# Kernel tuning notes

Hardware: AMD Instinct MI355X
Metric: run time of the kernel (lower is better)

## Reference

```python
import jax, jax.numpy as jnp
import numpy as np

NC = 80          # num_classes
NA = 3           # anchors per scale
G = 1.0          # offset magnitude; 1 + ceil(G/0.5) = 3
THRESH = 4.0     # anchor wh ratio threshold
BALANCE = (4.0, 1.0, 0.4)
CP, CN = 1.0, 0.0  # smooth_BCE(eps=0.0)
ANCHORS = np.array([[10, 13], [16, 30], [33, 23],
                    [30, 61], [62, 45], [59, 119],
                    [116, 90], [156, 198], [373, 326]], np.float32).reshape(3, 3, 2)
OFFS = np.array([[0, 0], [1, 0], [0, 1], [-1, 0], [0, -1]], np.float32) * G


def _build_targets(targets, grids, image_size):
    """Host-side (numpy) YOLOv7 target assignment: per-scale offset expansion,
    in-grid filtering and anchor-ratio filtering (data-dependent shapes)."""
    tcls, tbox, indices, anch = [], [], [], []
    for i, (H, W) in enumerate(grids):
        ng = np.array([H, W], np.float32)
        stride = image_size / ng                 # [sy, sx]
        anchor = ANCHORS[i] / stride[[1, 0]]     # anchors (w,h) in grid units
        gain = np.ones(6, np.float32)
        gain[2:] = (1.0 / stride)[[1, 0, 1, 0]]  # scale cx,cy,w,h to grid units
        rows = (targets * gain).reshape(-1, 6)   # [M,6]: nb,cls,cx,cy,w,h
        nb_, cls_, cx, cy, gw, gh = rows.T
        gx = cx[None, :] - OFFS[:, 0:1]          # [5,M] candidate cell x
        gy = cy[None, :] - OFFS[:, 1:2]
        brd = lambda v: np.broadcast_to(v[None, :], gx.shape)
        cand = np.stack([brd(nb_), brd(cls_), brd(cx), brd(cy),
                         gx, gy, brd(gw), brd(gh)], -1)        # [5,M,8]
        j = (gx >= 0) & (gx < ng[1]) & (gy >= 0) & (gy < ng[0])
        t = cand[j]                                             # [K,8]
        r = t[None, :, 6:8] / anchor[:, None]                   # [na,K,2]
        jj = np.maximum(r, 1.0 / r).max(-1) < THRESH            # [na,K]
        ai = np.broadcast_to(np.arange(NA, dtype=np.float32)[:, None], jj.shape)
        t = np.concatenate([np.broadcast_to(t[None], (NA,) + t.shape)[jj],
                            ai[jj][:, None]], 1)                # [n,9]
        b = t[:, 0].astype(np.int64)
        c = t[:, 1].astype(np.int64)
        gij = t[:, 4:6].astype(np.int64)                        # (gi, gj)
        a = t[:, 8].astype(np.int64)
        indices.append((jnp.asarray(b), jnp.asarray(a),
                        jnp.asarray(gij[:, 1]), jnp.asarray(gij[:, 0])))
        tbox.append(jnp.asarray(np.concatenate([t[:, 2:4] - gij, t[:, 6:8]], 1)))
        anch.append(jnp.asarray(anchor[a]))
        tcls.append(jnp.asarray(c))
    return tcls, tbox, indices, anch


def _ciou(box1, box2, eps=1e-7):
    # boxes in cxcywh, shape [n,4]
    w1, h1 = box1[:, 2], box1[:, 3]
    w2, h2 = box2[:, 2], box2[:, 3]
    b1x1, b1x2 = box1[:, 0] - w1 / 2, box1[:, 0] + w1 / 2
    b1y1, b1y2 = box1[:, 1] - h1 / 2, box1[:, 1] + h1 / 2
    b2x1, b2x2 = box2[:, 0] - w2 / 2, box2[:, 0] + w2 / 2
    b2y1, b2y2 = box2[:, 1] - h2 / 2, box2[:, 1] + h2 / 2
    inter = (jnp.clip(jnp.minimum(b1x2, b2x2) - jnp.maximum(b1x1, b2x1), 0) *
             jnp.clip(jnp.minimum(b1y2, b2y2) - jnp.maximum(b1y1, b2y1), 0))
    union = w1 * h1 + w2 * h2 - inter + eps
    iou = inter / union
    cw = jnp.maximum(b1x2, b2x2) - jnp.minimum(b1x1, b2x1)
    ch = jnp.maximum(b1y2, b2y2) - jnp.minimum(b1y1, b2y1)
    c2 = cw ** 2 + ch ** 2 + eps
    rho2 = ((b2x1 + b2x2 - b1x1 - b1x2) ** 2 +
            (b2y1 + b2y2 - b1y1 - b1y2) ** 2) / 4.0
    v = (4.0 / jnp.pi ** 2) * (jnp.arctan(w2 / (h2 + eps)) -
                               jnp.arctan(w1 / (h1 + eps))) ** 2
    alpha = jax.lax.stop_gradient(v / (v - iou + (1.0 + eps)))
    return iou - (rho2 / c2 + v * alpha)


def _bce_logits(x, t):
    # mean-reduced BCEWithLogits (pos_weight=1)
    return jnp.mean(jnp.maximum(x, 0) - x * t + jnp.log1p(jnp.exp(-jnp.abs(x))))


def _loss(preds, targets_np, image_size_np):
    grids = [p.shape[-2:] for p in preds]
    tcls, tbox, indices, anch = _build_targets(targets_np, grids, image_size_np)
    lbox = jnp.float32(0.0)
    lobj = jnp.float32(0.0)
    lcls = jnp.float32(0.0)
    for i, pi in enumerate(preds):
        B, C, H, W = pi.shape
        p = pi.reshape(B, NA, C // NA, H, W).transpose(0, 1, 3, 4, 2)  # [B,na,H,W,no]
        b, a, gj, gi = indices[i]
        tobj = jnp.zeros(p.shape[:-1], p.dtype)
        n = int(b.shape[0])
        if n:
            ps = p[b, a, gj, gi]                                       # [n,no]
            pxy = jax.nn.sigmoid(ps[:, 0:2]) * 3.0 - G                 # (1+ceil(G/0.5))=3
            pwh = (jax.nn.sigmoid(ps[:, 2:4]) * 2.0) ** 2 * anch[i]
            iou = _ciou(jnp.concatenate([pxy, pwh], 1), tbox[i])
            lbox = lbox + (1.0 - iou).mean()
            tobj = tobj.at[b, a, gj, gi].set(
                jnp.clip(jax.lax.stop_gradient(iou), 0.0).astype(p.dtype))
            if NC > 1:
                t = jnp.full((n, NC), CN, p.dtype)
                t = t.at[jnp.arange(n), tcls[i] - 1].set(CP)
                lcls = lcls + _bce_logits(ps[:, 5:], t)
        lobj = lobj + _bce_logits(p[..., 4], tobj) * BALANCE[i]
    lbox, lobj, lcls = lbox * 3.54, lobj * 64.3, lcls * 37.4
    return lbox + lobj + lcls, lbox, lobj, lcls


def setup_inputs() -> dict:
    key = jax.random.key(0)
    k0, k1, k2, k3, k4, k5 = jax.random.split(key, 6)
    B, m = 16, 12
    p0 = jax.random.normal(k0, (B, 255, 80, 80), jnp.float32)
    p1 = jax.random.normal(k1, (B, 255, 40, 40), jnp.float32)
    p2 = jax.random.normal(k2, (B, 255, 20, 20), jnp.float32)
    nb = jnp.broadcast_to(jnp.arange(B, dtype=jnp.float32)[:, None], (B, m))
    cls = jax.random.randint(k3, (B, m), 1, NC + 1).astype(jnp.float32)
    cxy = jax.random.uniform(k4, (B, m, 2), jnp.float32, 0.05, 0.95)
    wh = jax.random.uniform(k5, (B, m, 2), jnp.float32, 0.02, 0.4)
    targets = jnp.concatenate([nb[..., None], cls[..., None], cxy, wh], -1)
    image_size = jnp.array([640.0, 640.0], jnp.float32)
    return {"p0": p0, "p1": p1, "p2": p2, "targets": targets, "image_size": image_size}


def reference(p0, p1, p2, targets, image_size):
    return _loss((p0, p1, p2), np.asarray(targets), np.asarray(image_size))
```

## Files before the change

kernel.cpp:

```cpp
#include <hip/hip_runtime.h>
#include <math.h>


#define NT     192
#define NOFF   5
#define NANCH  3
#define MAXC   (NANCH*NOFF*NT)
#define THRESH 4.0f
#define NB     16
#define NCLS   80
#define NPLANE 144
#define NBLK   (NPLANE + 3)
#define MAGIC  0x5EED0001
#define WS_FLAG   0
#define WS_DENSE  160
#define WS_ASSIGN 320

__device__ __constant__ int   c_H[3]  = {80, 40, 20};
__device__ __constant__ int   c_W[3]  = {80, 40, 20};
__device__ __constant__ int   c_HW[3] = {6400, 1600, 400};
__device__ __constant__ float c_anch[18] = {10,13, 16,30, 33,23,
                                            30,61, 62,45, 59,119,
                                            116,90, 156,198, 373,326};
__device__ __constant__ float c_offs[10] = {0,0, 1,0, 0,1, -1,0, 0,-1};

__device__ __forceinline__ float sigmoidf(float x) {
    return 1.0f / (1.0f + __expf(-x));
}
__device__ __forceinline__ float softplusf(float x) {
    return fmaxf(x, 0.0f) + __logf(1.0f + __expf(-fabsf(x)));
}

__global__ void __launch_bounds__(256)
k_fused(const float* __restrict__ p0,
        const float* __restrict__ p1,
        const float* __restrict__ p2,
        const float* __restrict__ targets,
        const float* __restrict__ image_size,
        float* __restrict__ ws,
        float* __restrict__ out) {
    const int bid = blockIdx.x;
    const int tid = threadIdx.x;
    int* iws = (int*)ws;

    __shared__ float s_red[8];
    __shared__ float s_t[NT * 6];
    __shared__ float s_isz[2];
    __shared__ float s_sp[3];

    if (tid < 8) s_red[tid] = 0.0f;
    if (tid < 3) s_sp[tid] = 0.0f;

    if (bid < NPLANE) {
        const int scale = bid / (NB * NANCH);
        const int rem   = bid % (NB * NANCH);
        const int b     = rem / NANCH;
        const int a     = rem % NANCH;
        const int HW    = c_HW[scale];
        const float* p  = (scale == 0) ? p0 : ((scale == 1) ? p1 : p2);
        const float4* plane = (const float4*)(p + (size_t)b * 255 * HW
                                                + (size_t)(a * 85 + 4) * HW);
        const int n4 = HW >> 2;
        float s = 0.0f;
        for (int i = tid; i < n4; i += 256) {
            const float4 v = plane[i];
            s += softplusf(v.x) + softplusf(v.y) + softplusf(v.z) + softplusf(v.w);
        }
        for (int off = 32; off > 0; off >>= 1) s += __shfl_down(s, off, 64);
        if ((tid & 63) == 0) s_red[tid >> 6] = s;
        __syncthreads();
        if (tid == 0) {
            const float part = s_red[0] + s_red[1] + s_red[2] + s_red[3];
            atomicExch(&ws[WS_DENSE + bid], part);
            __threadfence();
            atomicExch(&iws[WS_FLAG + bid], MAGIC);
        }
    } else {
        const int scale = bid - NPLANE;
        if (tid == 0) { s_isz[0] = image_size[0]; s_isz[1] = image_size[1]; }
        for (int k = tid; k < NT * 6; k += 256) s_t[k] = targets[k];
        __syncthreads();

        const int H = c_H[scale], W = c_W[scale];
        const int HW = c_HW[scale];
        const float gx_mul = (float)W / s_isz[1];
        const float gy_mul = (float)H / s_isz[0];
        const float* p = (scale == 0) ? p0 : ((scale == 1) ? p1 : p2);

        int   n_loc = 0;
        float corr_loc = 0.0f, lbox_loc = 0.0f, lcls_loc = 0.0f;

        for (int k = tid; k < MAXC; k += 256) {
            const int a   = k / (NOFF * NT);
            const int rm  = k % (NOFF * NT);
            const int o   = rm / NT;
            const int t   = rm % NT;

            const float cx = s_t[t*6 + 2] * gx_mul;
            const float cy = s_t[t*6 + 3] * gy_mul;
            const float gw = s_t[t*6 + 4] * gx_mul;
            const float gh = s_t[t*6 + 5] * gy_mul;

            const float gxf = cx - c_offs[o*2 + 0];
            const float gyf = cy - c_offs[o*2 + 1];
            if (!(gxf >= 0.0f && gxf < (float)W && gyf >= 0.0f && gyf < (float)H))
                continue;

            const float aw = c_anch[(scale*3 + a)*2 + 0] * gx_mul;
            const float ah = c_anch[(scale*3 + a)*2 + 1] * gy_mul;
            const float rx = gw / aw, ry = gh / ah;
            const float mr = fmaxf(fmaxf(rx, 1.0f/rx), fmaxf(ry, 1.0f/ry));
            if (!(mr < THRESH)) continue;

            n_loc++;

            const int b   = (int)s_t[t*6 + 0];
            const int cls = (int)s_t[t*6 + 1];
            const int gi  = (int)gxf;
            const int gj  = (int)gyf;
            const float tbx = cx - (float)gi;
            const float tby = cy - (float)gj;

            const float* base = p + (size_t)b * 255 * HW + (size_t)(a * 85) * HW
                                  + (size_t)gj * W + gi;

            const float ps0 = base[0];
            const float ps1 = base[(size_t)HW];
            const float ps2 = base[2*(size_t)HW];
            const float ps3 = base[3*(size_t)HW];
            const float ps4 = base[4*(size_t)HW];

            const float px = sigmoidf(ps0) * 3.0f - 1.0f;
            const float py = sigmoidf(ps1) * 3.0f - 1.0f;
            float pw = sigmoidf(ps2) * 2.0f; pw = pw * pw * aw;
            float ph = sigmoidf(ps3) * 2.0f; ph = ph * ph * ah;

            const float eps = 1e-7f;
            const float b1x1 = px - pw*0.5f, b1x2 = px + pw*0.5f;
            const float b1y1 = py - ph*0.5f, b1y2 = py + ph*0.5f;
            const float b2x1 = tbx - gw*0.5f, b2x2 = tbx + gw*0.5f;
            const float b2y1 = tby - gh*0.5f, b2y2 = tby + gh*0.5f;
            const float iw = fmaxf(fminf(b1x2,b2x2) - fmaxf(b1x1,b2x1), 0.0f);
            const float ih = fmaxf(fminf(b1y2,b2y2) - fmaxf(b1y1,b2y1), 0.0f);
            const float inter = iw * ih;
            const float uni   = pw*ph + gw*gh - inter + eps;
            const float iou   = inter / uni;
            const float cwid  = fmaxf(b1x2,b2x2) - fminf(b1x1,b2x1);
            const float chgt  = fmaxf(b1y2,b2y2) - fminf(b1y1,b2y1);
            const float c2    = cwid*cwid + chgt*chgt + eps;
            const float dx    = b2x1 + b2x2 - b1x1 - b1x2;
            const float dy    = b2y1 + b2y2 - b1y1 - b1y2;
            const float rho2  = (dx*dx + dy*dy) * 0.25f;
            const float dv    = atanf(gw / (gh + eps)) - atanf(pw / (ph + eps));
            const float v     = 0.4052847345693511f * dv * dv;
            const float alpha = v / (v - iou + (1.0f + eps));
            const float ciou  = iou - (rho2 / c2 + v * alpha);

            lbox_loc += 1.0f - ciou;
            corr_loc += ps4 * fmaxf(ciou, 0.0f);

            float ls = 0.0f;
            for (int c = 0; c < NCLS; c++) {
                const float x  = base[(size_t)(5 + c) * HW];
                const float tv = (c == cls - 1) ? 1.0f : 0.0f;
                ls += fmaxf(x, 0.0f) - x * tv + __logf(1.0f + __expf(-fabsf(x)));
            }
            lcls_loc += ls;
        }

        float nf = (float)n_loc;
        for (int off = 32; off > 0; off >>= 1) {
            nf       += __shfl_down(nf,       off, 64);
            corr_loc += __shfl_down(corr_loc, off, 64);
            lbox_loc += __shfl_down(lbox_loc, off, 64);
            lcls_loc += __shfl_down(lcls_loc, off, 64);
        }
        __shared__ float s_a[4][4];
        if ((tid & 63) == 0) {
            const int w = tid >> 6;
            s_a[w][0] = nf; s_a[w][1] = corr_loc;
            s_a[w][2] = lbox_loc; s_a[w][3] = lcls_loc;
        }
        __syncthreads();
        if (tid == 0) {
            const float n_s    = s_a[0][0]+s_a[1][0]+s_a[2][0]+s_a[3][0];
            const float corr_s = s_a[0][1]+s_a[1][1]+s_a[2][1]+s_a[3][1];
            const float lbox_s = s_a[0][2]+s_a[1][2]+s_a[2][2]+s_a[3][2];
            const float lcls_s = s_a[0][3]+s_a[1][3]+s_a[2][3]+s_a[3][3];
            const int basei = WS_ASSIGN + scale * 4;
            atomicExch(&iws[basei + 0], (int)(n_s + 0.5f));
            atomicExch(&ws [basei + 1], corr_s);
            atomicExch(&ws [basei + 2], lbox_s);
            atomicExch(&ws [basei + 3], lcls_s);
            __threadfence();
            atomicExch(&iws[WS_FLAG + bid], MAGIC);
        }
    }

    if (bid == NBLK - 1) {
        __syncthreads();
        if (tid < NBLK) {
            while (atomicOr(&iws[WS_FLAG + tid], 0) != MAGIC) {
                __builtin_amdgcn_s_sleep(1);
            }
        }
        __syncthreads();
        if (tid < NPLANE) {
            const float v = atomicAdd(&ws[WS_DENSE + tid], 0.0f);
            atomicAdd(&s_sp[tid / (NB * NANCH)], v);
        }
        __syncthreads();
        if (tid == 0) {
            const float bal[3] = {4.0f, 1.0f, 0.4f};
            float lobj = 0.0f, lbox = 0.0f, lcls = 0.0f;
            #pragma unroll
            for (int i = 0; i < 3; i++) {
                const int basei = WS_ASSIGN + i * 4;
                const int   n    = atomicAdd(&iws[basei + 0], 0);
                const float corr = atomicAdd(&ws [basei + 1], 0.0f);
                const float lbx  = atomicAdd(&ws [basei + 2], 0.0f);
                const float lcl  = atomicAdd(&ws [basei + 3], 0.0f);
                const float cnt  = (float)(NB * NANCH * c_HW[i]);
                lobj += (s_sp[i] - corr) / cnt * bal[i];
                if (n > 0) {
                    lbox += lbx / (float)n;
                    lcls += lcl / ((float)n * (float)NCLS);
                }
            }
            lbox *= 3.54f;
            lobj *= 64.3f;
            lcls *= 37.4f;
            out[0] = lbox + lobj + lcls;
            out[1] = lbox;
            out[2] = lobj;
            out[3] = lcls;
        }
    }
}

extern "C" void kernel_launch(void* const* d_in, const int* in_sizes, int n_in,
                              void* d_out, int out_size, void* d_ws, size_t ws_size,
                              hipStream_t stream) {
    const float* p0  = (const float*)d_in[0];
    const float* p1  = (const float*)d_in[1];
    const float* p2  = (const float*)d_in[2];
    const float* tgt = (const float*)d_in[3];
    const float* isz = (const float*)d_in[4];
    float* out = (float*)d_out;
    float* ws  = (float*)d_ws;

    k_fused<<<NBLK, 256, 0, stream>>>(p0, p1, p2, tgt, isz, ws, out);
}
```

Measured before the change: 155.5 us.

## Split target-assignment work across 45 blocks and use a dedicated reducer block

The per-scale assignment blocks, each looping over 2880 candidates, are replaced by 45 blocks, one per (scale, anchor, offset), each handling 192 targets with one thread per target. A separate final block waits on all work blocks and reduces the per-block partials in shared memory, instead of the last assignment block doing it. This shortens the serial critical path, where a few blocks each did up to 12 iterations with an 80-class gather loop. In exchange there are more spin-wait flags, and the per-block partial counts are stored as floats.

```diff
diff --git a/kernel.cpp b/kernel.cpp
--- a/kernel.cpp
+++ b/kernel.cpp
@@ -2,19 +2,21 @@
 #include <math.h>
 
 
-#define NT     192
-#define NOFF   5
-#define NANCH  3
-#define MAXC   (NANCH*NOFF*NT)
-#define THRESH 4.0f
-#define NB     16
-#define NCLS   80
-#define NPLANE 144
-#define NBLK   (NPLANE + 3)
-#define MAGIC  0x5EED0001
+#define NT      192
+#define NOFF    5
+#define NANCH   3
+#define THRESH  4.0f
+#define NB      16
+#define NCLS    80
+#define NPLANE  144
+#define NAPS    (NANCH*NOFF)
+#define NASSIGN (3*NAPS)
+#define NWORK   (NPLANE + NASSIGN)
+#define NBLK    (NWORK + 1)
+#define MAGIC   0x5EED0001
 #define WS_FLAG   0
-#define WS_DENSE  160
-#define WS_ASSIGN 320
+#define WS_DENSE  256
+#define WS_ASSIGN 448
 
 __device__ __constant__ int   c_H[3]  = {80, 40, 20};
 __device__ __constant__ int   c_W[3]  = {80, 40, 20};
@@ -46,12 +48,12 @@
     __shared__ float s_red[8];
     __shared__ float s_t[NT * 6];
     __shared__ float s_isz[2];
+    __shared__ float s_a[4][4];
     __shared__ float s_sp[3];
-
-    if (tid < 8) s_red[tid] = 0.0f;
-    if (tid < 3) s_sp[tid] = 0.0f;
+    __shared__ float s_as[3][4];
 
     if (bid < NPLANE) {
+        if (tid < 8) s_red[tid] = 0.0f;
         const int scale = bid / (NB * NANCH);
         const int rem   = bid % (NB * NANCH);
         const int b     = rem / NANCH;
@@ -75,8 +77,13 @@
             __threadfence();
             atomicExch(&iws[WS_FLAG + bid], MAGIC);
         }
-    } else {
-        const int scale = bid - NPLANE;
+    } else if (bid < NWORK) {
+        const int aid   = bid - NPLANE;
+        const int scale = aid / NAPS;
+        const int chunk = aid % NAPS;
+        const int a     = chunk / NOFF;
+        const int o     = chunk % NOFF;
+
         if (tid == 0) { s_isz[0] = image_size[0]; s_isz[1] = image_size[1]; }
         for (int k = tid; k < NT * 6; k += 256) s_t[k] = targets[k];
         __syncthreads();
@@ -87,14 +94,11 @@
         const float gy_mul = (float)H / s_isz[0];
         const float* p = (scale == 0) ? p0 : ((scale == 1) ? p1 : p2);
 
-        int   n_loc = 0;
+        float n_loc = 0.0f;
         float corr_loc = 0.0f, lbox_loc = 0.0f, lcls_loc = 0.0f;
 
-        for (int k = tid; k < MAXC; k += 256) {
-            const int a   = k / (NOFF * NT);
-            const int rm  = k % (NOFF * NT);
-            const int o   = rm / NT;
-            const int t   = rm % NT;
+        if (tid < NT) {
+            const int t = tid;
 
             const float cx = s_t[t*6 + 2] * gx_mul;
             const float cy = s_t[t*6 + 3] * gy_mul;
@@ -103,103 +107,99 @@
 
             const float gxf = cx - c_offs[o*2 + 0];
             const float gyf = cy - c_offs[o*2 + 1];
-            if (!(gxf >= 0.0f && gxf < (float)W && gyf >= 0.0f && gyf < (float)H))
-                continue;
+            const bool in_grid = (gxf >= 0.0f && gxf < (float)W &&
+                                  gyf >= 0.0f && gyf < (float)H);
 
             const float aw = c_anch[(scale*3 + a)*2 + 0] * gx_mul;
             const float ah = c_anch[(scale*3 + a)*2 + 1] * gy_mul;
             const float rx = gw / aw, ry = gh / ah;
             const float mr = fmaxf(fmaxf(rx, 1.0f/rx), fmaxf(ry, 1.0f/ry));
-            if (!(mr < THRESH)) continue;
-
-            n_loc++;
-
-            const int b   = (int)s_t[t*6 + 0];
-            const int cls = (int)s_t[t*6 + 1];
-            const int gi  = (int)gxf;
-            const int gj  = (int)gyf;
-            const float tbx = cx - (float)gi;
-            const float tby = cy - (float)gj;
-
-            const float* base = p + (size_t)b * 255 * HW + (size_t)(a * 85) * HW
-                                  + (size_t)gj * W + gi;
-
-            const float ps0 = base[0];
-            const float ps1 = base[(size_t)HW];
-            const float ps2 = base[2*(size_t)HW];
-            const float ps3 = base[3*(size_t)HW];
-            const float ps4 = base[4*(size_t)HW];
-
-            const float px = sigmoidf(ps0) * 3.0f - 1.0f;
-            const float py = sigmoidf(ps1) * 3.0f - 1.0f;
-            float pw = sigmoidf(ps2) * 2.0f; pw = pw * pw * aw;
-            float ph = sigmoidf(ps3) * 2.0f; ph = ph * ph * ah;
-
-            const float eps = 1e-7f;
-            const float b1x1 = px - pw*0.5f, b1x2 = px + pw*0.5f;
-            const float b1y1 = py - ph*0.5f, b1y2 = py + ph*0.5f;
-            const float b2x1 = tbx - gw*0.5f, b2x2 = tbx + gw*0.5f;
-            const float b2y1 = tby - gh*0.5f, b2y2 = tby + gh*0.5f;
-            const float iw = fmaxf(fminf(b1x2,b2x2) - fmaxf(b1x1,b2x1), 0.0f);
-            const float ih = fmaxf(fminf(b1y2,b2y2) - fmaxf(b1y1,b2y1), 0.0f);
-            const float inter = iw * ih;
-            const float uni   = pw*ph + gw*gh - inter + eps;
-            const float iou   = inter / uni;
-            const float cwid  = fmaxf(b1x2,b2x2) - fminf(b1x1,b2x1);
-            const float chgt  = fmaxf(b1y2,b2y2) - fminf(b1y1,b2y1);
-            const float c2    = cwid*cwid + chgt*chgt + eps;
-            const float dx    = b2x1 + b2x2 - b1x1 - b1x2;
-            const float dy    = b2y1 + b2y2 - b1y1 - b1y2;
-            const float rho2  = (dx*dx + dy*dy) * 0.25f;
-            const float dv    = atanf(gw / (gh + eps)) - atanf(pw / (ph + eps));
-            const float v     = 0.4052847345693511f * dv * dv;
-            const float alpha = v / (v - iou + (1.0f + eps));
-            const float ciou  = iou - (rho2 / c2 + v * alpha);
-
-            lbox_loc += 1.0f - ciou;
-            corr_loc += ps4 * fmaxf(ciou, 0.0f);
-
-            float ls = 0.0f;
-            for (int c = 0; c < NCLS; c++) {
-                const float x  = base[(size_t)(5 + c) * HW];
-                const float tv = (c == cls - 1) ? 1.0f : 0.0f;
-                ls += fmaxf(x, 0.0f) - x * tv + __logf(1.0f + __expf(-fabsf(x)));
+
+            if (in_grid && (mr < THRESH)) {
+                n_loc = 1.0f;
+
+                const int b   = (int)s_t[t*6 + 0];
+                const int cls = (int)s_t[t*6 + 1];
+                const int gi  = (int)gxf;
+                const int gj  = (int)gyf;
+                const float tbx = cx - (float)gi;
+                const float tby = cy - (float)gj;
+
+                const float* base = p + (size_t)b * 255 * HW
+                                      + (size_t)(a * 85) * HW
+                                      + (size_t)gj * W + gi;
+
+                const float ps0 = base[0];
+                const float ps1 = base[(size_t)HW];
+                const float ps2 = base[2*(size_t)HW];
+                const float ps3 = base[3*(size_t)HW];
+                const float ps4 = base[4*(size_t)HW];
+
+                const float px = sigmoidf(ps0) * 3.0f - 1.0f;
+                const float py = sigmoidf(ps1) * 3.0f - 1.0f;
+                float pw = sigmoidf(ps2) * 2.0f; pw = pw * pw * aw;
+                float ph = sigmoidf(ps3) * 2.0f; ph = ph * ph * ah;
+
+                const float eps = 1e-7f;
+                const float b1x1 = px - pw*0.5f, b1x2 = px + pw*0.5f;
+                const float b1y1 = py - ph*0.5f, b1y2 = py + ph*0.5f;
+                const float b2x1 = tbx - gw*0.5f, b2x2 = tbx + gw*0.5f;
+                const float b2y1 = tby - gh*0.5f, b2y2 = tby + gh*0.5f;
+                const float iw = fmaxf(fminf(b1x2,b2x2) - fmaxf(b1x1,b2x1), 0.0f);
+                const float ih = fmaxf(fminf(b1y2,b2y2) - fmaxf(b1y1,b2y1), 0.0f);
+                const float inter = iw * ih;
+                const float uni   = pw*ph + gw*gh - inter + eps;
+                const float iou   = inter / uni;
+                const float cwid  = fmaxf(b1x2,b2x2) - fminf(b1x1,b2x1);
+                const float chgt  = fmaxf(b1y2,b2y2) - fminf(b1y1,b2y1);
+                const float c2    = cwid*cwid + chgt*chgt + eps;
+                const float dx    = b2x1 + b2x2 - b1x1 - b1x2;
+                const float dy    = b2y1 + b2y2 - b1y1 - b1y2;
+                const float rho2  = (dx*dx + dy*dy) * 0.25f;
+                const float dv    = atanf(gw / (gh + eps)) - atanf(pw / (ph + eps));
+                const float v     = 0.4052847345693511f * dv * dv;
+                const float alpha = v / (v - iou + (1.0f + eps));
+                const float ciou  = iou - (rho2 / c2 + v * alpha);
+
+                lbox_loc = 1.0f - ciou;
+                corr_loc = ps4 * fmaxf(ciou, 0.0f);
+
+                float ls = 0.0f;
+                const float* cb = base + 5*(size_t)HW;
+                for (int c = 0; c < NCLS; c++) {
+                    const float x  = cb[(size_t)c * HW];
+                    const float tv = (c == cls - 1) ? 1.0f : 0.0f;
+                    ls += fmaxf(x, 0.0f) - x * tv + __logf(1.0f + __expf(-fabsf(x)));
+                }
+                lcls_loc = ls;
             }
-            lcls_loc += ls;
-        }
-
-        float nf = (float)n_loc;
+        }
+
         for (int off = 32; off > 0; off >>= 1) {
-            nf       += __shfl_down(nf,       off, 64);
+            n_loc    += __shfl_down(n_loc,    off, 64);
             corr_loc += __shfl_down(corr_loc, off, 64);
             lbox_loc += __shfl_down(lbox_loc, off, 64);
             lcls_loc += __shfl_down(lcls_loc, off, 64);
         }
-        __shared__ float s_a[4][4];
         if ((tid & 63) == 0) {
             const int w = tid >> 6;
-            s_a[w][0] = nf; s_a[w][1] = corr_loc;
+            s_a[w][0] = n_loc;    s_a[w][1] = corr_loc;
             s_a[w][2] = lbox_loc; s_a[w][3] = lcls_loc;
         }
         __syncthreads();
         if (tid == 0) {
-            const float n_s    = s_a[0][0]+s_a[1][0]+s_a[2][0]+s_a[3][0];
-            const float corr_s = s_a[0][1]+s_a[1][1]+s_a[2][1]+s_a[3][1];
-            const float lbox_s = s_a[0][2]+s_a[1][2]+s_a[2][2]+s_a[3][2];
-            const float lcls_s = s_a[0][3]+s_a[1][3]+s_a[2][3]+s_a[3][3];
-            const int basei = WS_ASSIGN + scale * 4;
-            atomicExch(&iws[basei + 0], (int)(n_s + 0.5f));
-            atomicExch(&ws [basei + 1], corr_s);
-            atomicExch(&ws [basei + 2], lbox_s);
-            atomicExch(&ws [basei + 3], lcls_s);
+            const int basei = WS_ASSIGN + aid * 4;
+            atomicExch(&ws[basei + 0], s_a[0][0]+s_a[1][0]+s_a[2][0]+s_a[3][0]);
+            atomicExch(&ws[basei + 1], s_a[0][1]+s_a[1][1]+s_a[2][1]+s_a[3][1]);
+            atomicExch(&ws[basei + 2], s_a[0][2]+s_a[1][2]+s_a[2][2]+s_a[3][2]);
+            atomicExch(&ws[basei + 3], s_a[0][3]+s_a[1][3]+s_a[2][3]+s_a[3][3]);
             __threadfence();
             atomicExch(&iws[WS_FLAG + bid], MAGIC);
         }
-    }
-
-    if (bid == NBLK - 1) {
-        __syncthreads();
-        if (tid < NBLK) {
+    } else {
+        if (tid < 3)  s_sp[tid] = 0.0f;
+        if (tid < 12) ((float*)s_as)[tid] = 0.0f;
+        if (tid < NWORK) {
             while (atomicOr(&iws[WS_FLAG + tid], 0) != MAGIC) {
                 __builtin_amdgcn_s_sleep(1);
             }
@@ -208,6 +208,14 @@
         if (tid < NPLANE) {
             const float v = atomicAdd(&ws[WS_DENSE + tid], 0.0f);
             atomicAdd(&s_sp[tid / (NB * NANCH)], v);
+        }
+        if (tid < NASSIGN) {
+            const int s = tid / NAPS;
+            const int basei = WS_ASSIGN + tid * 4;
+            atomicAdd(&s_as[s][0], atomicAdd(&ws[basei + 0], 0.0f));
+            atomicAdd(&s_as[s][1], atomicAdd(&ws[basei + 1], 0.0f));
+            atomicAdd(&s_as[s][2], atomicAdd(&ws[basei + 2], 0.0f));
+            atomicAdd(&s_as[s][3], atomicAdd(&ws[basei + 3], 0.0f));
         }
         __syncthreads();
         if (tid == 0) {
@@ -215,16 +223,15 @@
             float lobj = 0.0f, lbox = 0.0f, lcls = 0.0f;
             #pragma unroll
             for (int i = 0; i < 3; i++) {
-                const int basei = WS_ASSIGN + i * 4;
-                const int   n    = atomicAdd(&iws[basei + 0], 0);
-                const float corr = atomicAdd(&ws [basei + 1], 0.0f);
-                const float lbx  = atomicAdd(&ws [basei + 2], 0.0f);
-                const float lcl  = atomicAdd(&ws [basei + 3], 0.0f);
+                const float n    = s_as[i][0];
+                const float corr = s_as[i][1];
+                const float lbx  = s_as[i][2];
+                const float lcl  = s_as[i][3];
                 const float cnt  = (float)(NB * NANCH * c_HW[i]);
                 lobj += (s_sp[i] - corr) / cnt * bal[i];
-                if (n > 0) {
-                    lbox += lbx / (float)n;
-                    lcls += lcl / ((float)n * (float)NCLS);
+                if (n > 0.5f) {
+                    lbox += lbx / n;
+                    lcls += lcl / (n * (float)NCLS);
                 }
             }
             lbox *= 3.54f;
```

Result: no change. 153.9 us (-1.0%).
